# Performance work log

Measured on AMD Instinct MI355X. Metric: run time of the kernel, lower is better.

## Reference

```python
import jax, jax.numpy as jnp
import numpy as np

N_NODES = 50000
N_EDGES = 600000
HID = 128
OUT = 14
LAYERS = 3
N_GRAPHS = 16
NODE_VOCAB = (120, 6)
EDGE_VOCAB = (6, 3)
GEN_EPS = 1e-7   # GENConv eps added after ReLU on messages
BN_EPS = 1e-5    # torch BatchNorm1d default eps


def setup_inputs() -> dict:
    key = jax.random.key(0)
    ks = jax.random.split(key, 14)
    inp = {}
    inp['node_feat0'] = jax.random.randint(ks[0], (N_NODES,), 0, NODE_VOCAB[0], dtype=jnp.int32)
    inp['node_feat1'] = jax.random.randint(ks[1], (N_NODES,), 0, NODE_VOCAB[1], dtype=jnp.int32)
    inp['edge_feat0'] = jax.random.randint(ks[2], (N_EDGES,), 0, EDGE_VOCAB[0], dtype=jnp.int32)
    inp['edge_feat1'] = jax.random.randint(ks[3], (N_EDGES,), 0, EDGE_VOCAB[1], dtype=jnp.int32)
    inp['edge_src'] = jax.random.randint(ks[4], (N_EDGES,), 0, N_NODES, dtype=jnp.int32)
    inp['edge_dst'] = jax.random.randint(ks[5], (N_EDGES,), 0, N_NODES, dtype=jnp.int32)
    inp['graph_ids'] = jnp.repeat(jnp.arange(N_GRAPHS, dtype=jnp.int32), N_NODES // N_GRAPHS)
    inp['num_graphs'] = N_GRAPHS
    s = 0.05
    inp['W_node0'] = jax.random.normal(ks[6], (NODE_VOCAB[0], HID), jnp.float32) * s
    inp['W_node1'] = jax.random.normal(ks[7], (NODE_VOCAB[1], HID), jnp.float32) * s
    # per-layer edge embedding tables (each GENConv layer has its own)
    inp['edge_emb0'] = jax.random.normal(ks[8], (LAYERS, EDGE_VOCAB[0], HID), jnp.float32) * s
    inp['edge_emb1'] = jax.random.normal(ks[9], (LAYERS, EDGE_VOCAB[1], HID), jnp.float32) * s
    inp['beta'] = jnp.ones((LAYERS,), jnp.float32)  # learnable softmax temperature, init 1.0
    inp['mlp_W'] = jax.random.normal(ks[10], (LAYERS, HID, HID), jnp.float32) * (1.0 / np.sqrt(HID))
    inp['mlp_b'] = jnp.zeros((LAYERS, HID), jnp.float32)
    inp['bn_gamma'] = jnp.ones((LAYERS, HID), jnp.float32)
    inp['bn_beta'] = jnp.zeros((LAYERS, HID), jnp.float32)
    inp['W_out'] = jax.random.normal(ks[11], (HID, OUT), jnp.float32) * (1.0 / np.sqrt(HID))
    inp['b_out'] = jnp.zeros((OUT,), jnp.float32)
    return inp


def _segment_softmax(z, seg, num_segments):
    # DGL edge_softmax: elementwise softmax over edges sharing a destination node.
    zmax = jax.ops.segment_max(z, seg, num_segments=num_segments)
    zmax = jnp.where(jnp.isfinite(zmax), zmax, 0.0)  # guard empty segments
    e = jnp.exp(z - zmax[seg])
    denom = jax.ops.segment_sum(e, seg, num_segments=num_segments)
    return e / denom[seg]


def reference(node_feat0, node_feat1, edge_feat0, edge_feat1, edge_src, edge_dst,
              graph_ids, num_graphs, W_node0, W_node1, edge_emb0, edge_emb1,
              beta, mlp_W, mlp_b, bn_gamma, bn_beta, W_out, b_out):
    # node embedding lookup + sum over tables
    hv = W_node0[node_feat0] + W_node1[node_feat1]          # [N, H]
    n = hv.shape[0]
    for l in range(mlp_W.shape[0]):
        # BatchNorm1d (training mode: batch stats, biased variance) + ReLU
        mu = jnp.mean(hv, axis=0)
        var = jnp.var(hv, axis=0)
        hv1 = (hv - mu) * jax.lax.rsqrt(var + BN_EPS) * bn_gamma[l] + bn_beta[l]
        hv1 = jax.nn.relu(hv1)
        # GENConv: edge embed sum, u_add_e, relu+eps, edge_softmax, scatter-sum
        ee = edge_emb0[l][edge_feat0] + edge_emb1[l][edge_feat1]   # [E, H]
        m = jax.nn.relu(hv1[edge_src] + ee) + GEN_EPS              # [E, H]
        a = _segment_softmax(m * beta[l], edge_dst, n)             # [E, H]
        agg = jax.ops.segment_sum(m * a, edge_dst, num_segments=n)  # [N, H]
        # feats = node_feats + msg, then 1-layer MLP, then outer skip connect
        hv = (hv1 + agg) @ mlp_W[l] + mlp_b[l] + hv
    # AvgPooling over each graph in the batch, then output Linear
    counts = jax.ops.segment_sum(jnp.ones((n,), hv.dtype), graph_ids, num_segments=num_graphs)
    hg = jax.ops.segment_sum(hv, graph_ids, num_segments=num_graphs) / counts[:, None]
    return hg @ W_out + b_out  # [num_graphs, OUT]
```

## Files before the change

kernel.cpp:

```cpp
#include <hip/hip_runtime.h>

#define N_NODESC 50000
#define N_EDGESC 600000
#define HID 128
#define LAYERS 3
#define N_GRAPHSC 16
#define OUT_DIM 14
#define GEN_EPS 1e-7f
#define BN_EPS 1e-5f
#define SCAN_BLK 196
#define POOL_BLK 400
#define EMB_BLK 6250
#define WF_BLK 192
#define GEMM_BLK 782
#define BNR_BLK 64
#define LOG2E 1.44269504f

typedef short bf16x8 __attribute__((ext_vector_type(8)));
typedef float f32x4 __attribute__((ext_vector_type(4)));

__device__ __forceinline__ unsigned short f2bf(float f) {
    union { float f; unsigned u; } v; v.f = f;
    unsigned r = v.u + 0x7FFF + ((v.u >> 16) & 1);
    return (unsigned short)(r >> 16);
}
__device__ __forceinline__ float bf_lo(unsigned u) {
    return __uint_as_float(u << 16);
}
__device__ __forceinline__ float bf_hi(unsigned u) {
    return __uint_as_float(u & 0xFFFF0000u);
}

__global__ void k_count(const int* __restrict__ dst, int* __restrict__ deg) {
    int i = blockIdx.x * blockDim.x + threadIdx.x;
    if (i < N_EDGESC) atomicAdd(&deg[dst[i]], 1);
}

__global__ void k_blocksum(const int* __restrict__ deg, int* __restrict__ part) {
    __shared__ int sh[256];
    int t = threadIdx.x;
    int i = blockIdx.x * 256 + t;
    sh[t] = (i < N_NODESC) ? deg[i] : 0;
    __syncthreads();
    for (int off = 128; off > 0; off >>= 1) {
        if (t < off) sh[t] += sh[t + off];
        __syncthreads();
    }
    if (t == 0) part[blockIdx.x] = sh[0];
}

__global__ void k_scanpart(const int* __restrict__ part, int* __restrict__ bofs) {
    __shared__ int sh[256];
    int t = threadIdx.x;
    int v = (t < SCAN_BLK) ? part[t] : 0;
    sh[t] = v;
    __syncthreads();
    for (int off = 1; off < 256; off <<= 1) {
        int add = (t >= off) ? sh[t - off] : 0;
        __syncthreads();
        sh[t] += add;
        __syncthreads();
    }
    if (t < SCAN_BLK) bofs[t] = sh[t] - v;
}

__global__ void k_rowptr(const int* __restrict__ deg, const int* __restrict__ bofs,
                         int* __restrict__ row_ptr, int* __restrict__ cursor) {
    __shared__ int sh[256];
    int t = threadIdx.x;
    int i = blockIdx.x * 256 + t;
    int d = (i < N_NODESC) ? deg[i] : 0;
    sh[t] = d;
    __syncthreads();
    for (int off = 1; off < 256; off <<= 1) {
        int add = (t >= off) ? sh[t - off] : 0;
        __syncthreads();
        sh[t] += add;
        __syncthreads();
    }
    if (i < N_NODESC) {
        int rp = bofs[blockIdx.x] + sh[t] - d;
        row_ptr[i] = rp;
        cursor[i] = rp;
    }
    if (i == 0) row_ptr[N_NODESC] = N_EDGESC;
}

__global__ void k_scatter(const int* __restrict__ dst, const int* __restrict__ src,
                          const int* __restrict__ f0, const int* __restrict__ f1,
                          int* __restrict__ cursor, int* __restrict__ csr_pack) {
    int i = blockIdx.x * blockDim.x + threadIdx.x;
    if (i < N_EDGESC) {
        int pos = atomicAdd(&cursor[dst[i]], 1);
        csr_pack[pos] = (src[i] << 8) | ((f0[i] * 3 + f1[i]) * 8);
    }
}

__global__ void k_embed(const int* __restrict__ f0, const int* __restrict__ f1,
                        const float4* __restrict__ W0, const float4* __restrict__ W1,
                        float4* __restrict__ hv4, float* __restrict__ part,
                        const float* __restrict__ W, unsigned short* __restrict__ wf) {
    int tid = threadIdx.x;
    if (blockIdx.x >= EMB_BLK) {
        int i = (blockIdx.x - EMB_BLK) * 256 + tid;
        if (i < LAYERS * 4 * 8 * 64 * 8) {
            int j = i & 7;
            int lane = (i >> 3) & 63;
            int nt = (i >> 9) & 7;
            int ks = (i >> 12) & 3;
            int l = i >> 14;
            int k = ks * 32 + (lane >> 4) * 8 + j;
            int n = nt * 16 + (lane & 15);
            wf[i] = f2bf(W[(size_t)l * HID * HID + k * HID + n]);
        }
        return;
    }
    __shared__ float sh[1024], sh2[1024];
    int i = blockIdx.x * 256 + tid;
    int v = i >> 5, c4 = i & 31;
    float4 a = W0[f0[v] * 32 + c4];
    float4 b = W1[f1[v] * 32 + c4];
    float4 o = make_float4(a.x + b.x, a.y + b.y, a.z + b.z, a.w + b.w);
    hv4[i] = o;
    sh[tid * 4 + 0] = o.x; sh2[tid * 4 + 0] = o.x * o.x;
    sh[tid * 4 + 1] = o.y; sh2[tid * 4 + 1] = o.y * o.y;
    sh[tid * 4 + 2] = o.z; sh2[tid * 4 + 2] = o.z * o.z;
    sh[tid * 4 + 3] = o.w; sh2[tid * 4 + 3] = o.w * o.w;
    __syncthreads();
    if (tid < 128) {
        int c4i = tid >> 2, j = tid & 3;
        float s = 0.f, s2 = 0.f;
#pragma unroll
        for (int r = 0; r < 8; r++) {
            s += sh[(r * 32 + c4i) * 4 + j];
            s2 += sh2[(r * 32 + c4i) * 4 + j];
        }
        part[(size_t)blockIdx.x * 256 + tid] = s;
        part[(size_t)blockIdx.x * 256 + 128 + tid] = s2;
    }
}

__global__ void k_bn_reduce2(const float* __restrict__ part, int nparts,
                             float* __restrict__ gsum) {
    int t = threadIdx.x;
    int rows = (nparts + BNR_BLK - 1) / BNR_BLK;
    int r0 = blockIdx.x * rows;
    int r1 = min(r0 + rows, nparts);
    float s = 0.f;
    for (int p = r0; p < r1; p++) s += part[(size_t)p * 256 + t];
    atomicAdd(&gsum[t], s);
}

__global__ void k_hv1b(const float4* __restrict__ hv4, const float* __restrict__ gsum,
                       const float* __restrict__ gamma, const float* __restrict__ betab,
                       uint2* __restrict__ hv1b) {
    int i = blockIdx.x * 256 + threadIdx.x;
    int c = (i & 31) * 4;
    const float invN = 1.f / (float)N_NODESC;
    float4 h = hv4[i];
    float r[4];
#pragma unroll
    for (int j = 0; j < 4; j++) {
        float mu = gsum[c + j] * invN;
        float var = gsum[128 + c + j] * invN - mu * mu;
        float sc = gamma[c + j] * rsqrtf(var + BN_EPS);
        float sf = betab[c + j] - mu * sc;
        r[j] = fmaxf(fmaf((&h.x)[j], sc, sf), 0.f);
    }
    uint2 o;
    o.x = (unsigned)f2bf(r[0]) | ((unsigned)f2bf(r[1]) << 16);
    o.y = (unsigned)f2bf(r[2]) | ((unsigned)f2bf(r[3]) << 16);
    hv1b[i] = o;
}

__global__ __launch_bounds__(512) void k_aggemm(
    const unsigned* __restrict__ hv1b, const int* __restrict__ row_ptr,
    const int* __restrict__ csr_pack, const float* __restrict__ e0,
    const float* __restrict__ e1, const float* __restrict__ beta_p,
    const unsigned short* __restrict__ wf, const float* __restrict__ b,
    float* __restrict__ hv, float* __restrict__ part) {
    __shared__ float2 sh_et[18 * 64];
    __shared__ unsigned x_tile[64 * 64];
    __shared__ float shs[512], shs2[512];
    int tid = threadIdx.x;
    for (int i = tid; i < 18 * 64; i += 512) {
        int f = i >> 6, ln = i & 63;
        int a = f / 3, bb = f - 3 * a;
        float2 ea = *(const float2*)(e0 + a * HID + 2 * ln);
        float2 eb = *(const float2*)(e1 + bb * HID + 2 * ln);
        sh_et[i] = make_float2(ea.x + eb.x, ea.y + eb.y);
    }
    int w = tid >> 6, lane = tid & 63;
    int m0 = blockIdx.x * 64;
    float beta = *beta_p;
    const float bl2 = beta * LOG2E;
    __syncthreads();

    const char* hv1c = (const char*)hv1b;
    const char* etc = (const char*)sh_et;
    unsigned lane4 = (unsigned)lane * 4;
    unsigned lane8 = (unsigned)lane * 8;

#define AGG_BODY(J)                                                         \
    {                                                                       \
        int pack = __shfl(pk, (J), 64);                                     \
        unsigned u = *(const unsigned*)(hv1c +                              \
                        ((((unsigned)pack) & 0xFFFFFF00u) + lane4));        \
        float2 t = *(const float2*)(etc +                                   \
                        (((((unsigned)pack) & 0xFFu) << 6) + lane8));       \
        float r0 = fmaxf(bf_lo(u) + t.x, 0.f);                              \
        float r1 = fmaxf(bf_hi(u) + t.y, 0.f);                              \
        float w0 = exp2f(r0 * bl2);                                         \
        float w1 = exp2f(r1 * bl2);                                         \
        d0 += w0; d1 += w1;                                                 \
        n0 = fmaf(r0, w0, n0); n1 = fmaf(r1, w1, n1);                       \
    }

    for (int i = 0; i < 8; i++) {
        int row = w * 8 + i;
        int v = m0 + row;
        int vc = min(v, N_NODESC - 1);
        unsigned su = hv1b[(size_t)vc * 64 + lane];
        int p0 = row_ptr[vc];
        int deg = (v < N_NODESC) ? (row_ptr[vc + 1] - p0) : 0;
        float n0 = 0.f, n1 = 0.f, d0 = 0.f, d1 = 0.f;
        for (int base = 0; base < deg; base += 64) {
            int idx = base + lane;
            int pk = (idx < deg) ? csr_pack[p0 + idx] : 0;
            int jn = min(64, deg - base);
            int j = 0;
            for (; j + 2 <= jn; j += 2) {
                AGG_BODY(j)
                AGG_BODY(j + 1)
            }
            if (j < jn) AGG_BODY(j)
        }
        float ox = bf_lo(su) + (deg ? __fdividef(n0, d0) + GEN_EPS : 0.f);
        float oy = bf_hi(su) + (deg ? __fdividef(n1, d1) + GEN_EPS : 0.f);
        x_tile[row * 64 + ((lane + row * 4) & 63)] =
            (unsigned)f2bf(ox) | ((unsigned)f2bf(oy) << 16);
    }
#undef AGG_BODY
    __syncthreads();

    int rw = w & 3, chh = w >> 2;
    int mrow = lane & 15, grp = lane >> 4;
    int rbase = rw * 16 + mrow;
    bf16x8 af[4];
#pragma unroll
    for (int ks = 0; ks < 4; ks++) {
        int col = ks * 16 + grp * 4;
        int colr = (col + rbase * 4) & 63;
        af[ks] = *(const bf16x8*)&x_tile[rbase * 64 + colr];
    }
    f32x4 acc[4];
#pragma unroll
    for (int nt = 0; nt < 4; nt++) acc[nt] = (f32x4){0.f, 0.f, 0.f, 0.f};
#pragma unroll
    for (int nt = 0; nt < 4; nt++) {
        int ntg = chh * 4 + nt;
#pragma unroll
        for (int ks = 0; ks < 4; ks++) {
            bf16x8 bfr = *(const bf16x8*)(wf + (size_t)((ks * 8 + ntg) * 64 + lane) * 8);
            acc[nt] = __builtin_amdgcn_mfma_f32_16x16x32_bf16(af[ks], bfr, acc[nt], 0, 0, 0);
        }
    }
#pragma unroll
    for (int nt = 0; nt < 4; nt++) {
        int col = chh * 64 + nt * 16 + mrow;
        float bias = b[col];
        float s = 0.f, s2 = 0.f;
#pragma unroll
        for (int r = 0; r < 4; r++) {
            int v = m0 + rw * 16 + grp * 4 + r;
            if (v < N_NODESC) {
                size_t idx = (size_t)v * HID + col;
                float o = acc[nt][r] + bias + hv[idx];
                hv[idx] = o;
                s += o; s2 += o * o;
            }
        }
        s  += __shfl_xor(s, 16, 64);  s  += __shfl_xor(s, 32, 64);
        s2 += __shfl_xor(s2, 16, 64); s2 += __shfl_xor(s2, 32, 64);
        if (lane < 16) { shs[rw * 128 + col] = s; shs2[rw * 128 + col] = s2; }
    }
    __syncthreads();
    if (tid < 128) {
        part[(size_t)blockIdx.x * 256 + tid] =
            shs[tid] + shs[128 + tid] + shs[256 + tid] + shs[384 + tid];
    } else if (tid < 256) {
        int c = tid - 128;
        part[(size_t)blockIdx.x * 256 + tid] =
            shs2[c] + shs2[128 + c] + shs2[256 + c] + shs2[384 + c];
    }
}

__global__ void k_pool(const float* __restrict__ hv, float* __restrict__ part2) {
    int tid = threadIdx.x;
    int c = tid & 127, rh = tid >> 7;
    int start = blockIdx.x * 125;
    float acc = 0.f;
    for (int r = start + rh; r < start + 125; r += 2)
        acc += hv[(size_t)r * HID + c];
    __shared__ float sh[256];
    sh[tid] = acc;
    __syncthreads();
    if (rh == 0) part2[blockIdx.x * 128 + c] = acc + sh[tid + 128];
}

__global__ void k_finish(const float* __restrict__ part2, const float* __restrict__ Wo,
                         const float* __restrict__ bo, float* __restrict__ out) {
    __shared__ float hg[N_GRAPHSC * HID];
    int t = threadIdx.x;
    for (int s = t; s < N_GRAPHSC * HID; s += 256) {
        int g = s >> 7, c = s & 127;
        float x = 0.f;
#pragma unroll
        for (int i = 0; i < 25; i++) x += part2[(g * 25 + i) * 128 + c];
        hg[s] = x;
    }
    __syncthreads();
    if (t < N_GRAPHSC * OUT_DIM) {
        int g = t / OUT_DIM, o = t % OUT_DIM;
        const float inv = (float)N_GRAPHSC / (float)N_NODESC;
        float acc = bo[o];
        for (int k = 0; k < HID; k++)
            acc += hg[g * HID + k] * inv * Wo[k * OUT_DIM + o];
        out[t] = acc;
    }
}

extern "C" void kernel_launch(void* const* d_in, const int* in_sizes, int n_in,
                              void* d_out, int out_size, void* d_ws, size_t ws_size,
                              hipStream_t stream) {
    const int* node_feat0 = (const int*)d_in[0];
    const int* node_feat1 = (const int*)d_in[1];
    const int* edge_feat0 = (const int*)d_in[2];
    const int* edge_feat1 = (const int*)d_in[3];
    const int* edge_src   = (const int*)d_in[4];
    const int* edge_dst   = (const int*)d_in[5];
    const float* W_node0   = (const float*)d_in[8];
    const float* W_node1   = (const float*)d_in[9];
    const float* edge_emb0 = (const float*)d_in[10];
    const float* edge_emb1 = (const float*)d_in[11];
    const float* beta      = (const float*)d_in[12];
    const float* mlp_W     = (const float*)d_in[13];
    const float* mlp_b     = (const float*)d_in[14];
    const float* bn_gamma  = (const float*)d_in[15];
    const float* bn_beta   = (const float*)d_in[16];
    const float* W_out     = (const float*)d_in[17];
    const float* b_out     = (const float*)d_in[18];
    float* out = (float*)d_out;

    char* ws = (char*)d_ws;
    size_t off = 0;
    auto alloc = [&](size_t bytes) -> void* {
        void* p = ws + off;
        off += (bytes + 255) & ~(size_t)255;
        return p;
    };
    float* hv      = (float*)alloc((size_t)N_NODESC * HID * 4);
    unsigned* hv1b = (unsigned*)alloc((size_t)N_NODESC * 64 * 4);
    float* bnpart  = (float*)alloc((size_t)EMB_BLK * 256 * 4);
    float* gsums   = (float*)alloc(LAYERS * 256 * 4);
    unsigned short* wfrag = (unsigned short*)alloc((size_t)LAYERS * 16384 * 2);
    float* part2   = (float*)alloc(POOL_BLK * 128 * 4);
    int* row_ptr   = (int*)alloc((N_NODESC + 1) * 4);
    int* cursor    = (int*)alloc(N_NODESC * 4);
    int* deg       = (int*)alloc(N_NODESC * 4);
    int* part      = (int*)alloc(SCAN_BLK * 4);
    int* bofs      = (int*)alloc(SCAN_BLK * 4);
    int* csr_pack  = (int*)alloc((size_t)N_EDGESC * 4);

    hipMemsetAsync(deg, 0, N_NODESC * 4, stream);
    hipMemsetAsync(gsums, 0, LAYERS * 256 * 4, stream);
    k_count<<<(N_EDGESC + 255) / 256, 256, 0, stream>>>(edge_dst, deg);
    k_blocksum<<<SCAN_BLK, 256, 0, stream>>>(deg, part);
    k_scanpart<<<1, 256, 0, stream>>>(part, bofs);
    k_rowptr<<<SCAN_BLK, 256, 0, stream>>>(deg, bofs, row_ptr, cursor);
    k_scatter<<<(N_EDGESC + 255) / 256, 256, 0, stream>>>(
        edge_dst, edge_src, edge_feat0, edge_feat1, cursor, csr_pack);

    k_embed<<<EMB_BLK + WF_BLK, 256, 0, stream>>>(
        node_feat0, node_feat1, (const float4*)W_node0, (const float4*)W_node1,
        (float4*)hv, bnpart, mlp_W, wfrag);

    for (int l = 0; l < LAYERS; l++) {
        float* gsum = gsums + l * 256;
        int nparts = (l == 0) ? EMB_BLK : GEMM_BLK;
        k_bn_reduce2<<<BNR_BLK, 256, 0, stream>>>(bnpart, nparts, gsum);
        k_hv1b<<<(N_NODESC * 32) / 256, 256, 0, stream>>>(
            (const float4*)hv, gsum, bn_gamma + l * HID, bn_beta + l * HID,
            (uint2*)hv1b);
        k_aggemm<<<GEMM_BLK, 512, 0, stream>>>(
            hv1b, row_ptr, csr_pack,
            edge_emb0 + (size_t)l * 6 * HID, edge_emb1 + (size_t)l * 3 * HID,
            beta + l, wfrag + (size_t)l * 16384, mlp_b + l * HID, hv, bnpart);
    }

    k_pool<<<POOL_BLK, 256, 0, stream>>>(hv, part2);
    k_finish<<<1, 256, 0, stream>>>(part2, W_out, b_out, out);
}
```

Before: 454.2 us.

## Store residual node state in bf16 and fuse BN stats via atomics

The persistent node state hv is now kept in bf16 instead of fp32, which halves the traffic of the residual read-modify-write in the aggregation+GEMM kernel and of the loads in the BN-apply and pooling kernels. The per-block BatchNorm partial sums for the next layer are atomically added straight into the global sums, so the separate reduction launch is dropped for layers after the first. The cost is bf16 rounding error in the residual stream, which compounds over layers, plus atomic contention on 256 addresses from 782 blocks.

```diff
diff --git a/kernel.cpp b/kernel.cpp
--- a/kernel.cpp
+++ b/kernel.cpp
@@ -30,6 +30,9 @@
 __device__ __forceinline__ float bf_hi(unsigned u) {
     return __uint_as_float(u & 0xFFFF0000u);
 }
+__device__ __forceinline__ float bfs(unsigned short u) {
+    return __uint_as_float(((unsigned)u) << 16);
+}
 
 __global__ void k_count(const int* __restrict__ dst, int* __restrict__ deg) {
     int i = blockIdx.x * blockDim.x + threadIdx.x;
@@ -98,7 +101,7 @@
 
 __global__ void k_embed(const int* __restrict__ f0, const int* __restrict__ f1,
                         const float4* __restrict__ W0, const float4* __restrict__ W1,
-                        float4* __restrict__ hv4, float* __restrict__ part,
+                        uint2* __restrict__ hvb2, float* __restrict__ part,
                         const float* __restrict__ W, unsigned short* __restrict__ wf) {
     int tid = threadIdx.x;
     if (blockIdx.x >= EMB_BLK) {
@@ -121,7 +124,10 @@
     float4 a = W0[f0[v] * 32 + c4];
     float4 b = W1[f1[v] * 32 + c4];
     float4 o = make_float4(a.x + b.x, a.y + b.y, a.z + b.z, a.w + b.w);
-    hv4[i] = o;
+    uint2 ob;
+    ob.x = (unsigned)f2bf(o.x) | ((unsigned)f2bf(o.y) << 16);
+    ob.y = (unsigned)f2bf(o.z) | ((unsigned)f2bf(o.w) << 16);
+    hvb2[i] = ob;
     sh[tid * 4 + 0] = o.x; sh2[tid * 4 + 0] = o.x * o.x;
     sh[tid * 4 + 1] = o.y; sh2[tid * 4 + 1] = o.y * o.y;
     sh[tid * 4 + 2] = o.z; sh2[tid * 4 + 2] = o.z * o.z;
@@ -151,13 +157,14 @@
     atomicAdd(&gsum[t], s);
 }
 
-__global__ void k_hv1b(const float4* __restrict__ hv4, const float* __restrict__ gsum,
+__global__ void k_hv1b(const uint2* __restrict__ hvb2, const float* __restrict__ gsum,
                        const float* __restrict__ gamma, const float* __restrict__ betab,
                        uint2* __restrict__ hv1b) {
     int i = blockIdx.x * 256 + threadIdx.x;
     int c = (i & 31) * 4;
     const float invN = 1.f / (float)N_NODESC;
-    float4 h = hv4[i];
+    uint2 hb = hvb2[i];
+    float h[4] = {bf_lo(hb.x), bf_hi(hb.x), bf_lo(hb.y), bf_hi(hb.y)};
     float r[4];
 #pragma unroll
     for (int j = 0; j < 4; j++) {
@@ -165,7 +172,7 @@
         float var = gsum[128 + c + j] * invN - mu * mu;
         float sc = gamma[c + j] * rsqrtf(var + BN_EPS);
         float sf = betab[c + j] - mu * sc;
-        r[j] = fmaxf(fmaf((&h.x)[j], sc, sf), 0.f);
+        r[j] = fmaxf(fmaf(h[j], sc, sf), 0.f);
     }
     uint2 o;
     o.x = (unsigned)f2bf(r[0]) | ((unsigned)f2bf(r[1]) << 16);
@@ -178,7 +185,7 @@
     const int* __restrict__ csr_pack, const float* __restrict__ e0,
     const float* __restrict__ e1, const float* __restrict__ beta_p,
     const unsigned short* __restrict__ wf, const float* __restrict__ b,
-    float* __restrict__ hv, float* __restrict__ part) {
+    unsigned short* __restrict__ hvb, float* __restrict__ gsum_next) {
     __shared__ float2 sh_et[18 * 64];
     __shared__ unsigned x_tile[64 * 64];
     __shared__ float shs[512], shs2[512];
@@ -275,8 +282,8 @@
             int v = m0 + rw * 16 + grp * 4 + r;
             if (v < N_NODESC) {
                 size_t idx = (size_t)v * HID + col;
-                float o = acc[nt][r] + bias + hv[idx];
-                hv[idx] = o;
+                float o = acc[nt][r] + bias + bfs(hvb[idx]);
+                hvb[idx] = f2bf(o);
                 s += o; s2 += o * o;
             }
         }
@@ -284,24 +291,27 @@
         s2 += __shfl_xor(s2, 16, 64); s2 += __shfl_xor(s2, 32, 64);
         if (lane < 16) { shs[rw * 128 + col] = s; shs2[rw * 128 + col] = s2; }
     }
-    __syncthreads();
-    if (tid < 128) {
-        part[(size_t)blockIdx.x * 256 + tid] =
-            shs[tid] + shs[128 + tid] + shs[256 + tid] + shs[384 + tid];
-    } else if (tid < 256) {
-        int c = tid - 128;
-        part[(size_t)blockIdx.x * 256 + tid] =
-            shs2[c] + shs2[128 + c] + shs2[256 + c] + shs2[384 + c];
-    }
-}
-
-__global__ void k_pool(const float* __restrict__ hv, float* __restrict__ part2) {
+    if (gsum_next) {
+        __syncthreads();
+        if (tid < 128) {
+            atomicAdd(&gsum_next[tid],
+                shs[tid] + shs[128 + tid] + shs[256 + tid] + shs[384 + tid]);
+        } else if (tid < 256) {
+            int c = tid - 128;
+            atomicAdd(&gsum_next[tid],
+                shs2[c] + shs2[128 + c] + shs2[256 + c] + shs2[384 + c]);
+        }
+    }
+}
+
+__global__ void k_pool(const unsigned short* __restrict__ hvb,
+                       float* __restrict__ part2) {
     int tid = threadIdx.x;
     int c = tid & 127, rh = tid >> 7;
     int start = blockIdx.x * 125;
     float acc = 0.f;
     for (int r = start + rh; r < start + 125; r += 2)
-        acc += hv[(size_t)r * HID + c];
+        acc += bfs(hvb[(size_t)r * HID + c]);
     __shared__ float sh[256];
     sh[tid] = acc;
     __syncthreads();
@@ -359,7 +369,7 @@
         off += (bytes + 255) & ~(size_t)255;
         return p;
     };
-    float* hv      = (float*)alloc((size_t)N_NODESC * HID * 4);
+    unsigned short* hvb = (unsigned short*)alloc((size_t)N_NODESC * HID * 2);
     unsigned* hv1b = (unsigned*)alloc((size_t)N_NODESC * 64 * 4);
     float* bnpart  = (float*)alloc((size_t)EMB_BLK * 256 * 4);
     float* gsums   = (float*)alloc(LAYERS * 256 * 4);
@@ -383,21 +393,21 @@
 
     k_embed<<<EMB_BLK + WF_BLK, 256, 0, stream>>>(
         node_feat0, node_feat1, (const float4*)W_node0, (const float4*)W_node1,
-        (float4*)hv, bnpart, mlp_W, wfrag);
+        (uint2*)hvb, bnpart, mlp_W, wfrag);
+    k_bn_reduce2<<<BNR_BLK, 256, 0, stream>>>(bnpart, EMB_BLK, gsums);
 
     for (int l = 0; l < LAYERS; l++) {
         float* gsum = gsums + l * 256;
-        int nparts = (l == 0) ? EMB_BLK : GEMM_BLK;
-        k_bn_reduce2<<<BNR_BLK, 256, 0, stream>>>(bnpart, nparts, gsum);
+        float* gnext = (l + 1 < LAYERS) ? gsums + (l + 1) * 256 : nullptr;
         k_hv1b<<<(N_NODESC * 32) / 256, 256, 0, stream>>>(
-            (const float4*)hv, gsum, bn_gamma + l * HID, bn_beta + l * HID,
+            (const uint2*)hvb, gsum, bn_gamma + l * HID, bn_beta + l * HID,
             (uint2*)hv1b);
         k_aggemm<<<GEMM_BLK, 512, 0, stream>>>(
             hv1b, row_ptr, csr_pack,
             edge_emb0 + (size_t)l * 6 * HID, edge_emb1 + (size_t)l * 3 * HID,
-            beta + l, wfrag + (size_t)l * 16384, mlp_b + l * HID, hv, bnpart);
-    }
-
-    k_pool<<<POOL_BLK, 256, 0, stream>>>(hv, part2);
+            beta + l, wfrag + (size_t)l * 16384, mlp_b + l * HID, hvb, gnext);
+    }
+
+    k_pool<<<POOL_BLK, 256, 0, stream>>>(hvb, part2);
     k_finish<<<1, 256, 0, stream>>>(part2, W_out, b_out, out);
 }
```

After: 463.4 us. 2.0% more time.
